# Kernel optimization log

Hardware: AMD Instinct MI355X
Metric: run time of the kernel (lower is better)

Reference implementation:

```python
import jax, jax.numpy as jnp
import numpy as np

N_VAR = 100000
N_CON = 100000
N_EDGE = 2000000
C = 32  # all channel widths


def _linear(x, W, b):
    return x @ W.T + b


def setup_inputs() -> dict:
    key = jax.random.key(0)
    ks = jax.random.split(key, 16)
    s = 1.0 / np.sqrt(C)
    se = 1.0 / np.sqrt(3 * C)
    inp = {
        "var_f": jax.random.normal(ks[0], (N_VAR, C), jnp.float32),
        "con_f": jax.random.normal(ks[1], (N_CON, C), jnp.float32),
        "combined_edge_f": jax.random.normal(ks[2], (N_EDGE, C), jnp.float32),
        "edge_index_var_con": jax.random.randint(ks[3], (2, N_EDGE), 0, N_VAR, jnp.int32),
        # var_compress_mlp
        "Wv1": jax.random.uniform(ks[4], (C, C), jnp.float32, -s, s),
        "bv1": jnp.zeros((C,), jnp.float32),
        "Wv2": jax.random.uniform(ks[5], (C, C), jnp.float32, -s, s),
        "bv2": jnp.zeros((C,), jnp.float32),
        # con_compress_mlp
        "Wc1": jax.random.uniform(ks[6], (C, C), jnp.float32, -s, s),
        "bc1": jnp.zeros((C,), jnp.float32),
        "Wc2": jax.random.uniform(ks[7], (C, C), jnp.float32, -s, s),
        "bc2": jnp.zeros((C,), jnp.float32),
        # edge_mlp (input width = 3*C)
        "We1": jax.random.uniform(ks[8], (C, 3 * C), jnp.float32, -se, se),
        "be1": jnp.zeros((C,), jnp.float32),
        "We2": jax.random.uniform(ks[9], (C, C), jnp.float32, -s, s),
        "be2": jnp.zeros((C,), jnp.float32),
    }
    return inp


def reference(var_f, con_f, combined_edge_f, edge_index_var_con,
              Wv1, bv1, Wv2, bv2, Wc1, bc1, Wc2, bc2, We1, be1, We2, be2):
    # compress node features with 2-layer ReLU MLPs (done on nodes, not edges)
    v = jax.nn.relu(_linear(jax.nn.relu(_linear(var_f, Wv1, bv1)), Wv2, bv2))
    c = jax.nn.relu(_linear(jax.nn.relu(_linear(con_f, Wc1, bc1)), Wc2, bc2))
    # gather per-edge and concat: [E, 3C]
    out = jnp.concatenate(
        [combined_edge_f, v[edge_index_var_con[0]], c[edge_index_var_con[1]]], axis=1)
    # edge MLP: Linear -> ReLU -> Linear (no final ReLU)
    return _linear(jax.nn.relu(_linear(out, We1, be1)), We2, be2)
```

## Files before the change

### kernel.cpp

```cpp
#include <hip/hip_runtime.h>

typedef float  f32x2  __attribute__((ext_vector_type(2)));
typedef float  f32x4  __attribute__((ext_vector_type(4)));
typedef float  f32x16 __attribute__((ext_vector_type(16)));
typedef short  s16x4  __attribute__((ext_vector_type(4)));
typedef short  s16x8  __attribute__((ext_vector_type(8)));
typedef unsigned int u32x2 __attribute__((ext_vector_type(2)));

__device__ __forceinline__ unsigned f2bf(float f) {
    unsigned u = __builtin_bit_cast(unsigned, f);
    u += 0x7FFFu + ((u >> 16) & 1u);
    return u >> 16;
}
__device__ __forceinline__ s16x4 pack4(float a, float b, float c, float d) {
    u32x2 u;
    u[0] = f2bf(a) | (f2bf(b) << 16);
    u[1] = f2bf(c) | (f2bf(d) << 16);
    return __builtin_bit_cast(s16x4, u);
}
__device__ __forceinline__ s16x4 pack4v(f32x4 v) { return pack4(v[0], v[1], v[2], v[3]); }
__device__ __forceinline__ s16x4 lo4(s16x8 v) { return __builtin_shufflevector(v, v, 0, 1, 2, 3); }
__device__ __forceinline__ s16x4 hi4(s16x8 v) { return __builtin_shufflevector(v, v, 4, 5, 6, 7); }

__device__ __forceinline__ void node_body(
    const float* __restrict__ X,
    const float* __restrict__ W1, const float* __restrict__ b1,
    const float* __restrict__ W2, const float* __restrict__ b2,
    const float* __restrict__ Wm, const float* __restrict__ bm,
    unsigned short* __restrict__ outp, int N, int tile0)
{
    const int lane = threadIdx.x & 63;
    const int g = lane >> 5, m = lane & 31;
    const int ntile = (N + 31) >> 5;
    if (tile0 >= ntile) return;

    s16x4 a1[4], a2[4], am[4];
#pragma unroll
    for (int q = 0; q < 4; ++q) {
        const float* p1 = W1 + m * 32 + 8 * q + 4 * g;
        a1[q] = pack4(p1[0], p1[1], p1[2], p1[3]);
        const float* p2 = W2 + m * 32 + 8 * q + 4 * g;
        a2[q] = pack4(p2[0], p2[1], p2[2], p2[3]);
        const float* pm = Wm + m * 96 + 8 * q + 4 * g;
        am[q] = pack4(pm[0], pm[1], pm[2], pm[3]);
    }
    f32x16 f1, f2, f3;
#pragma unroll
    for (int r = 0; r < 16; ++r) {
        int ch = (r & 3) + 8 * (r >> 2) + 4 * g;
        f1[r] = b1[ch];
        f2[r] = b2[ch];
        f3[r] = bm ? bm[ch] : 0.f;
    }

#pragma unroll
    for (int k = 0; k < 4; ++k) {
        const int tile = tile0 + k;
        if (tile >= ntile) break;
        const int node0 = tile * 32 + m;
        const int node = node0 < N ? node0 : N - 1;

        s16x4 bX[4];
#pragma unroll
        for (int q = 0; q < 4; ++q) {
            f32x4 v = *reinterpret_cast<const f32x4*>(X + (size_t)node * 32 + 8 * q + 4 * g);
            bX[q] = pack4v(v);
        }
        f32x16 acc = f1;
#pragma unroll
        for (int q = 0; q < 4; ++q) acc = __builtin_amdgcn_mfma_f32_32x32x8bf16_1k(a1[q], bX[q], acc, 0, 0, 0);
        s16x4 bH[4];
#pragma unroll
        for (int q = 0; q < 4; ++q)
            bH[q] = pack4(fmaxf(acc[4*q+0], 0.f), fmaxf(acc[4*q+1], 0.f),
                          fmaxf(acc[4*q+2], 0.f), fmaxf(acc[4*q+3], 0.f));
        acc = f2;
#pragma unroll
        for (int q = 0; q < 4; ++q) acc = __builtin_amdgcn_mfma_f32_32x32x8bf16_1k(a2[q], bH[q], acc, 0, 0, 0);
#pragma unroll
        for (int q = 0; q < 4; ++q)
            bH[q] = pack4(fmaxf(acc[4*q+0], 0.f), fmaxf(acc[4*q+1], 0.f),
                          fmaxf(acc[4*q+2], 0.f), fmaxf(acc[4*q+3], 0.f));
        acc = f3;
#pragma unroll
        for (int q = 0; q < 4; ++q) acc = __builtin_amdgcn_mfma_f32_32x32x8bf16_1k(am[q], bH[q], acc, 0, 0, 0);

        if (node0 < N) {
#pragma unroll
            for (int q = 0; q < 4; ++q) {
                s16x4 o = pack4(acc[4*q+0], acc[4*q+1], acc[4*q+2], acc[4*q+3]);
                *reinterpret_cast<s16x4*>(outp + (size_t)node0 * 32 + 8 * q + 4 * g) = o;
            }
        }
    }
}

__global__ __launch_bounds__(256) void nodes_kernel(
    const float* __restrict__ var_f, const float* __restrict__ con_f,
    const float* __restrict__ Wv1, const float* __restrict__ bv1,
    const float* __restrict__ Wv2, const float* __restrict__ bv2,
    const float* __restrict__ Wc1, const float* __restrict__ bc1,
    const float* __restrict__ Wc2, const float* __restrict__ bc2,
    const float* __restrict__ We1, const float* __restrict__ be1,
    unsigned short* __restrict__ pv, unsigned short* __restrict__ pc,
    int nV, int nC, int wavesV)
{
    const int wvg = (blockIdx.x * blockDim.x + threadIdx.x) >> 6;
    if (wvg < wavesV) {
        node_body(var_f, Wv1, bv1, Wv2, bv2, We1 + 32, be1, pv, nV, wvg * 4);
    } else {
        node_body(con_f, Wc1, bc1, Wc2, bc2, We1 + 64, nullptr, pc, nC,
                  (wvg - wavesV) * 4);
    }
}

__global__ __launch_bounds__(256, 4) void edge_kernel(
    const float* __restrict__ Ef, const int* __restrict__ idx,
    const unsigned short* __restrict__ pv, const unsigned short* __restrict__ pc,
    const float* __restrict__ We1, const float* __restrict__ We2,
    const float* __restrict__ be2,
    float* __restrict__ out, int nE)
{
    const int lane = threadIdx.x & 63;
    const int m = lane & 15, c = lane >> 4;

    s16x4 aW1[2][2], aP[2][2], aW2[2][2];
    f32x4 b2f[2];
#pragma unroll
    for (int r = 0; r < 2; ++r) {
#pragma unroll
        for (int kk = 0; kk < 2; ++kk) {
            const float* p1 = We1 + (16 * r + m) * 96 + 16 * kk + 4 * c;
            aW1[r][kk] = pack4(p1[0], p1[1], p1[2], p1[3]);
            const float* p2 = We2 + (16 * r + m) * 32 + 16 * kk + 4 * c;
            aW2[r][kk] = pack4(p2[0], p2[1], p2[2], p2[3]);
            const int j_hit = 16 * r + m - 8 * c - 4 * kk;
            s16x4 w;
#pragma unroll
            for (int j = 0; j < 4; ++j) w[j] = (short)((j == j_hit) ? 0x3F80 : 0);
            aP[r][kk] = w;
        }
        f32x4 b;
#pragma unroll
        for (int j = 0; j < 4; ++j) b[j] = be2[16 * r + 4 * c + j];
        b2f[r] = b;
    }

    const int ntile = nE >> 5;
    const int nw = (gridDim.x * blockDim.x) >> 6;
    int t = (blockIdx.x * blockDim.x + threadIdx.x) >> 6;
    if (t >= ntile) return;

    int ib0[2], ib1[2];
    s16x4 ebf[2][2];
    s16x8 pvf[2], pcf[2];
    {
        int i0[2], i1[2];
#pragma unroll
        for (int e = 0; e < 2; ++e) {
            i0[e] = idx[t * 32 + 16 * e + m];
            i1[e] = idx[nE + t * 32 + 16 * e + m];
        }
#pragma unroll
        for (int e = 0; e < 2; ++e) {
#pragma unroll
            for (int kk = 0; kk < 2; ++kk) {
                f32x4 v = *reinterpret_cast<const f32x4*>(
                    Ef + (size_t)(t * 32 + 16 * e + m) * 32 + 16 * kk + 4 * c);
                ebf[e][kk] = pack4v(v);
            }
            pvf[e] = *reinterpret_cast<const s16x8*>(pv + (size_t)i0[e] * 32 + 8 * c);
            pcf[e] = *reinterpret_cast<const s16x8*>(pc + (size_t)i1[e] * 32 + 8 * c);
        }
        int t1 = (t + nw < ntile) ? t + nw : t;
#pragma unroll
        for (int e = 0; e < 2; ++e) {
            ib0[e] = idx[t1 * 32 + 16 * e + m];
            ib1[e] = idx[nE + t1 * 32 + 16 * e + m];
        }
    }

    while (true) {
        const int tn = t + nw;
        const int tc = tn < ntile ? tn : t;

        f32x4 nef[2][2];
        s16x8 npv[2], npc[2];
        int ic0[2], ic1[2];
#pragma unroll
        for (int e = 0; e < 2; ++e) {
#pragma unroll
            for (int kk = 0; kk < 2; ++kk)
                nef[e][kk] = *reinterpret_cast<const f32x4*>(
                    Ef + (size_t)(tc * 32 + 16 * e + m) * 32 + 16 * kk + 4 * c);
            npv[e] = *reinterpret_cast<const s16x8*>(pv + (size_t)ib0[e] * 32 + 8 * c);
            npc[e] = *reinterpret_cast<const s16x8*>(pc + (size_t)ib1[e] * 32 + 8 * c);
        }
        {
            int t2 = (tn + nw < ntile) ? tn + nw : tc;
#pragma unroll
            for (int e = 0; e < 2; ++e) {
                ic0[e] = idx[t2 * 32 + 16 * e + m];
                ic1[e] = idx[nE + t2 * 32 + 16 * e + m];
            }
        }

        f32x4 a00 = {}, a01 = {}, a10 = {}, a11 = {};
        a00 = __builtin_amdgcn_mfma_f32_16x16x16bf16_1k(aW1[0][0], ebf[0][0], a00, 0, 0, 0);
        a01 = __builtin_amdgcn_mfma_f32_16x16x16bf16_1k(aW1[0][0], ebf[1][0], a01, 0, 0, 0);
        a10 = __builtin_amdgcn_mfma_f32_16x16x16bf16_1k(aW1[1][0], ebf[0][0], a10, 0, 0, 0);
        a11 = __builtin_amdgcn_mfma_f32_16x16x16bf16_1k(aW1[1][0], ebf[1][0], a11, 0, 0, 0);
        a00 = __builtin_amdgcn_mfma_f32_16x16x16bf16_1k(aW1[0][1], ebf[0][1], a00, 0, 0, 0);
        a01 = __builtin_amdgcn_mfma_f32_16x16x16bf16_1k(aW1[0][1], ebf[1][1], a01, 0, 0, 0);
        a10 = __builtin_amdgcn_mfma_f32_16x16x16bf16_1k(aW1[1][1], ebf[0][1], a10, 0, 0, 0);
        a11 = __builtin_amdgcn_mfma_f32_16x16x16bf16_1k(aW1[1][1], ebf[1][1], a11, 0, 0, 0);
        a00 = __builtin_amdgcn_mfma_f32_16x16x16bf16_1k(aP[0][0], lo4(pvf[0]), a00, 0, 0, 0);
        a00 = __builtin_amdgcn_mfma_f32_16x16x16bf16_1k(aP[0][1], hi4(pvf[0]), a00, 0, 0, 0);
        a01 = __builtin_amdgcn_mfma_f32_16x16x16bf16_1k(aP[0][0], lo4(pvf[1]), a01, 0, 0, 0);
        a01 = __builtin_amdgcn_mfma_f32_16x16x16bf16_1k(aP[0][1], hi4(pvf[1]), a01, 0, 0, 0);
        a10 = __builtin_amdgcn_mfma_f32_16x16x16bf16_1k(aP[1][0], lo4(pvf[0]), a10, 0, 0, 0);
        a10 = __builtin_amdgcn_mfma_f32_16x16x16bf16_1k(aP[1][1], hi4(pvf[0]), a10, 0, 0, 0);
        a11 = __builtin_amdgcn_mfma_f32_16x16x16bf16_1k(aP[1][0], lo4(pvf[1]), a11, 0, 0, 0);
        a11 = __builtin_amdgcn_mfma_f32_16x16x16bf16_1k(aP[1][1], hi4(pvf[1]), a11, 0, 0, 0);
        a00 = __builtin_amdgcn_mfma_f32_16x16x16bf16_1k(aP[0][0], lo4(pcf[0]), a00, 0, 0, 0);
        a00 = __builtin_amdgcn_mfma_f32_16x16x16bf16_1k(aP[0][1], hi4(pcf[0]), a00, 0, 0, 0);
        a01 = __builtin_amdgcn_mfma_f32_16x16x16bf16_1k(aP[0][0], lo4(pcf[1]), a01, 0, 0, 0);
        a01 = __builtin_amdgcn_mfma_f32_16x16x16bf16_1k(aP[0][1], hi4(pcf[1]), a01, 0, 0, 0);
        a10 = __builtin_amdgcn_mfma_f32_16x16x16bf16_1k(aP[1][0], lo4(pcf[0]), a10, 0, 0, 0);
        a10 = __builtin_amdgcn_mfma_f32_16x16x16bf16_1k(aP[1][1], hi4(pcf[0]), a10, 0, 0, 0);
        a11 = __builtin_amdgcn_mfma_f32_16x16x16bf16_1k(aP[1][0], lo4(pcf[1]), a11, 0, 0, 0);
        a11 = __builtin_amdgcn_mfma_f32_16x16x16bf16_1k(aP[1][1], hi4(pcf[1]), a11, 0, 0, 0);

        s16x4 bH00 = pack4(fmaxf(a00[0], 0.f), fmaxf(a00[1], 0.f), fmaxf(a00[2], 0.f), fmaxf(a00[3], 0.f));
        s16x4 bH01 = pack4(fmaxf(a10[0], 0.f), fmaxf(a10[1], 0.f), fmaxf(a10[2], 0.f), fmaxf(a10[3], 0.f));
        s16x4 bH10 = pack4(fmaxf(a01[0], 0.f), fmaxf(a01[1], 0.f), fmaxf(a01[2], 0.f), fmaxf(a01[3], 0.f));
        s16x4 bH11 = pack4(fmaxf(a11[0], 0.f), fmaxf(a11[1], 0.f), fmaxf(a11[2], 0.f), fmaxf(a11[3], 0.f));

        f32x4 o00 = b2f[0], o01 = b2f[0], o10 = b2f[1], o11 = b2f[1];
        o00 = __builtin_amdgcn_mfma_f32_16x16x16bf16_1k(aW2[0][0], bH00, o00, 0, 0, 0);
        o01 = __builtin_amdgcn_mfma_f32_16x16x16bf16_1k(aW2[0][0], bH10, o01, 0, 0, 0);
        o10 = __builtin_amdgcn_mfma_f32_16x16x16bf16_1k(aW2[1][0], bH00, o10, 0, 0, 0);
        o11 = __builtin_amdgcn_mfma_f32_16x16x16bf16_1k(aW2[1][0], bH10, o11, 0, 0, 0);
        o00 = __builtin_amdgcn_mfma_f32_16x16x16bf16_1k(aW2[0][1], bH01, o00, 0, 0, 0);
        o01 = __builtin_amdgcn_mfma_f32_16x16x16bf16_1k(aW2[0][1], bH11, o01, 0, 0, 0);
        o10 = __builtin_amdgcn_mfma_f32_16x16x16bf16_1k(aW2[1][1], bH01, o10, 0, 0, 0);
        o11 = __builtin_amdgcn_mfma_f32_16x16x16bf16_1k(aW2[1][1], bH11, o11, 0, 0, 0);

        {
            float* obase = out + (size_t)(t * 32) * 32;
            __builtin_nontemporal_store(o00, reinterpret_cast<f32x4*>(obase + (16 * 0 + m) * 32 + 16 * 0 + 4 * c));
            __builtin_nontemporal_store(o10, reinterpret_cast<f32x4*>(obase + (16 * 0 + m) * 32 + 16 * 1 + 4 * c));
            __builtin_nontemporal_store(o01, reinterpret_cast<f32x4*>(obase + (16 * 1 + m) * 32 + 16 * 0 + 4 * c));
            __builtin_nontemporal_store(o11, reinterpret_cast<f32x4*>(obase + (16 * 1 + m) * 32 + 16 * 1 + 4 * c));
        }

        if (tn >= ntile) break;
        t = tn;
#pragma unroll
        for (int e = 0; e < 2; ++e) {
#pragma unroll
            for (int kk = 0; kk < 2; ++kk) ebf[e][kk] = pack4v(nef[e][kk]);
            pvf[e] = npv[e]; pcf[e] = npc[e];
            ib0[e] = ic0[e]; ib1[e] = ic1[e];
        }
    }
}

extern "C" void kernel_launch(void* const* d_in, const int* in_sizes, int n_in,
                              void* d_out, int out_size, void* d_ws, size_t ws_size,
                              hipStream_t stream) {
    const float* var_f = (const float*)d_in[0];
    const float* con_f = (const float*)d_in[1];
    const float* Ef    = (const float*)d_in[2];
    const int*   idx   = (const int*)d_in[3];
    const float* Wv1 = (const float*)d_in[4];
    const float* bv1 = (const float*)d_in[5];
    const float* Wv2 = (const float*)d_in[6];
    const float* bv2 = (const float*)d_in[7];
    const float* Wc1 = (const float*)d_in[8];
    const float* bc1 = (const float*)d_in[9];
    const float* Wc2 = (const float*)d_in[10];
    const float* bc2 = (const float*)d_in[11];
    const float* We1 = (const float*)d_in[12];
    const float* be1 = (const float*)d_in[13];
    const float* We2 = (const float*)d_in[14];
    const float* be2 = (const float*)d_in[15];
    float* out = (float*)d_out;

    const int nV = in_sizes[0] / 32;
    const int nC = in_sizes[1] / 32;
    const int nE = in_sizes[2] / 32;

    unsigned short* pv = (unsigned short*)d_ws;
    unsigned short* pc = pv + (size_t)nV * 32;

    const int wavesV = (((nV + 31) >> 5) + 3) >> 2;
    const int wavesC = (((nC + 31) >> 5) + 3) >> 2;
    const int nodeBlocks = (wavesV + wavesC + 3) / 4;
    nodes_kernel<<<nodeBlocks, 256, 0, stream>>>(
        var_f, con_f, Wv1, bv1, Wv2, bv2, Wc1, bc1, Wc2, bc2,
        We1, be1, pv, pc, nV, nC, wavesV);

    edge_kernel<<<2048, 256, 0, stream>>>(Ef, idx, pv, pc, We1, We2, be2, out, nE);
}
```

Baseline: 176.3 us.

## Double-buffer edge tile prefetch two deep and stage output through LDS

The edge loop is restructured into two alternating register buffer sets, so feature and gather loads are issued two tiles ahead and index loads four tiles ahead, instead of one tile ahead. Output tiles are transposed through a padded per-wave LDS buffer so each lane writes contiguous 16-byte chunks of full rows rather than scattered fragments. The grid is halved to 1024 blocks. In exchange, register pressure rises from the doubled live prefetch state and LDS traffic is added. With fewer blocks there may be less latency hiding across waves.

After: 167.2 us. -5.2%, faster.

```diff
diff --git a/kernel.cpp b/kernel.cpp
--- a/kernel.cpp
+++ b/kernel.cpp
@@ -114,6 +114,92 @@
     }
 }
 
+#define EDGE_PHASE(P_ef00, P_ef01, P_ef10, P_ef11, P_pv0, P_pv1, P_pc0, P_pc1, \
+                   IX00, IX01, IX10, IX11, tcur)                               \
+    {                                                                          \
+        const int t_ = (tcur);                                                 \
+         \
+        s16x4 eb00 = pack4v(P_ef00), eb01 = pack4v(P_ef01);                    \
+        s16x4 eb10 = pack4v(P_ef10), eb11 = pack4v(P_ef11);                    \
+        f32x4 a00 = {}, a01 = {}, a10 = {}, a11 = {};                          \
+        a00 = __builtin_amdgcn_mfma_f32_16x16x16bf16_1k(aW1[0][0], eb00, a00, 0, 0, 0); \
+        a01 = __builtin_amdgcn_mfma_f32_16x16x16bf16_1k(aW1[0][0], eb10, a01, 0, 0, 0); \
+        a10 = __builtin_amdgcn_mfma_f32_16x16x16bf16_1k(aW1[1][0], eb00, a10, 0, 0, 0); \
+        a11 = __builtin_amdgcn_mfma_f32_16x16x16bf16_1k(aW1[1][0], eb10, a11, 0, 0, 0); \
+        a00 = __builtin_amdgcn_mfma_f32_16x16x16bf16_1k(aW1[0][1], eb01, a00, 0, 0, 0); \
+        a01 = __builtin_amdgcn_mfma_f32_16x16x16bf16_1k(aW1[0][1], eb11, a01, 0, 0, 0); \
+        a10 = __builtin_amdgcn_mfma_f32_16x16x16bf16_1k(aW1[1][1], eb01, a10, 0, 0, 0); \
+        a11 = __builtin_amdgcn_mfma_f32_16x16x16bf16_1k(aW1[1][1], eb11, a11, 0, 0, 0); \
+        a00 = __builtin_amdgcn_mfma_f32_16x16x16bf16_1k(aP[0][0], lo4(P_pv0), a00, 0, 0, 0); \
+        a00 = __builtin_amdgcn_mfma_f32_16x16x16bf16_1k(aP[0][1], hi4(P_pv0), a00, 0, 0, 0); \
+        a01 = __builtin_amdgcn_mfma_f32_16x16x16bf16_1k(aP[0][0], lo4(P_pv1), a01, 0, 0, 0); \
+        a01 = __builtin_amdgcn_mfma_f32_16x16x16bf16_1k(aP[0][1], hi4(P_pv1), a01, 0, 0, 0); \
+        a10 = __builtin_amdgcn_mfma_f32_16x16x16bf16_1k(aP[1][0], lo4(P_pv0), a10, 0, 0, 0); \
+        a10 = __builtin_amdgcn_mfma_f32_16x16x16bf16_1k(aP[1][1], hi4(P_pv0), a10, 0, 0, 0); \
+        a11 = __builtin_amdgcn_mfma_f32_16x16x16bf16_1k(aP[1][0], lo4(P_pv1), a11, 0, 0, 0); \
+        a11 = __builtin_amdgcn_mfma_f32_16x16x16bf16_1k(aP[1][1], hi4(P_pv1), a11, 0, 0, 0); \
+        a00 = __builtin_amdgcn_mfma_f32_16x16x16bf16_1k(aP[0][0], lo4(P_pc0), a00, 0, 0, 0); \
+        a00 = __builtin_amdgcn_mfma_f32_16x16x16bf16_1k(aP[0][1], hi4(P_pc0), a00, 0, 0, 0); \
+        a01 = __builtin_amdgcn_mfma_f32_16x16x16bf16_1k(aP[0][0], lo4(P_pc1), a01, 0, 0, 0); \
+        a01 = __builtin_amdgcn_mfma_f32_16x16x16bf16_1k(aP[0][1], hi4(P_pc1), a01, 0, 0, 0); \
+        a10 = __builtin_amdgcn_mfma_f32_16x16x16bf16_1k(aP[1][0], lo4(P_pc0), a10, 0, 0, 0); \
+        a10 = __builtin_amdgcn_mfma_f32_16x16x16bf16_1k(aP[1][1], hi4(P_pc0), a10, 0, 0, 0); \
+        a11 = __builtin_amdgcn_mfma_f32_16x16x16bf16_1k(aP[1][0], lo4(P_pc1), a11, 0, 0, 0); \
+        a11 = __builtin_amdgcn_mfma_f32_16x16x16bf16_1k(aP[1][1], hi4(P_pc1), a11, 0, 0, 0); \
+        s16x4 bH00 = pack4(fmaxf(a00[0], 0.f), fmaxf(a00[1], 0.f), fmaxf(a00[2], 0.f), fmaxf(a00[3], 0.f)); \
+        s16x4 bH01 = pack4(fmaxf(a10[0], 0.f), fmaxf(a10[1], 0.f), fmaxf(a10[2], 0.f), fmaxf(a10[3], 0.f)); \
+        s16x4 bH10 = pack4(fmaxf(a01[0], 0.f), fmaxf(a01[1], 0.f), fmaxf(a01[2], 0.f), fmaxf(a01[3], 0.f)); \
+        s16x4 bH11 = pack4(fmaxf(a11[0], 0.f), fmaxf(a11[1], 0.f), fmaxf(a11[2], 0.f), fmaxf(a11[3], 0.f)); \
+        f32x4 o00 = b2f[0], o01 = b2f[0], o10 = b2f[1], o11 = b2f[1];          \
+        o00 = __builtin_amdgcn_mfma_f32_16x16x16bf16_1k(aW2[0][0], bH00, o00, 0, 0, 0); \
+        o01 = __builtin_amdgcn_mfma_f32_16x16x16bf16_1k(aW2[0][0], bH10, o01, 0, 0, 0); \
+        o10 = __builtin_amdgcn_mfma_f32_16x16x16bf16_1k(aW2[1][0], bH00, o10, 0, 0, 0); \
+        o11 = __builtin_amdgcn_mfma_f32_16x16x16bf16_1k(aW2[1][0], bH10, o11, 0, 0, 0); \
+        o00 = __builtin_amdgcn_mfma_f32_16x16x16bf16_1k(aW2[0][1], bH01, o00, 0, 0, 0); \
+        o01 = __builtin_amdgcn_mfma_f32_16x16x16bf16_1k(aW2[0][1], bH11, o01, 0, 0, 0); \
+        o10 = __builtin_amdgcn_mfma_f32_16x16x16bf16_1k(aW2[1][1], bH01, o10, 0, 0, 0); \
+        o11 = __builtin_amdgcn_mfma_f32_16x16x16bf16_1k(aW2[1][1], bH11, o11, 0, 0, 0); \
+         \
+        {                                                                      \
+            int tf = t_ + 2 * nw; if (tf >= ntile) tf = ntile - 1;             \
+            P_ef00 = *reinterpret_cast<const f32x4*>(Ef + (size_t)(tf * 32 + m) * 32 + 4 * c); \
+            P_ef01 = *reinterpret_cast<const f32x4*>(Ef + (size_t)(tf * 32 + m) * 32 + 16 + 4 * c); \
+            P_ef10 = *reinterpret_cast<const f32x4*>(Ef + (size_t)(tf * 32 + 16 + m) * 32 + 4 * c); \
+            P_ef11 = *reinterpret_cast<const f32x4*>(Ef + (size_t)(tf * 32 + 16 + m) * 32 + 16 + 4 * c); \
+            P_pv0 = *reinterpret_cast<const s16x8*>(pv + (size_t)IX00 * 32 + 8 * c); \
+            P_pv1 = *reinterpret_cast<const s16x8*>(pv + (size_t)IX01 * 32 + 8 * c); \
+            P_pc0 = *reinterpret_cast<const s16x8*>(pc + (size_t)IX10 * 32 + 8 * c); \
+            P_pc1 = *reinterpret_cast<const s16x8*>(pc + (size_t)IX11 * 32 + 8 * c); \
+            int ti = t_ + 4 * nw; if (ti >= ntile) ti = ntile - 1;             \
+            IX00 = idx[ti * 32 + m];        IX01 = idx[ti * 32 + 16 + m];      \
+            IX10 = idx[nE + ti * 32 + m];   IX11 = idx[nE + ti * 32 + 16 + m]; \
+        }                                                                      \
+                \
+        {                                                                      \
+            float* p_ = ldsw + (size_t)m * 34 + 4 * c;                         \
+            *reinterpret_cast<f32x2*>(p_)      = f32x2{o00[0], o00[1]};        \
+            *reinterpret_cast<f32x2*>(p_ + 2)  = f32x2{o00[2], o00[3]};        \
+            *reinterpret_cast<f32x2*>(p_ + 16) = f32x2{o10[0], o10[1]};        \
+            *reinterpret_cast<f32x2*>(p_ + 18) = f32x2{o10[2], o10[3]};        \
+            float* q_ = ldsw + (size_t)(16 + m) * 34 + 4 * c;                  \
+            *reinterpret_cast<f32x2*>(q_)      = f32x2{o01[0], o01[1]};        \
+            *reinterpret_cast<f32x2*>(q_ + 2)  = f32x2{o01[2], o01[3]};        \
+            *reinterpret_cast<f32x2*>(q_ + 16) = f32x2{o11[0], o11[1]};        \
+            *reinterpret_cast<f32x2*>(q_ + 18) = f32x2{o11[2], o11[3]};        \
+            float* obase = out + (size_t)t_ * 1024;                            \
+            _Pragma("unroll")                                                  \
+            for (int p = 0; p < 4; ++p) {                                      \
+                int li = p * 256 + lane * 4;                                   \
+                int row = li >> 5, col = li & 31;                              \
+                const float* s_ = ldsw + (size_t)row * 34 + col;               \
+                f32x2 lo_ = *reinterpret_cast<const f32x2*>(s_);               \
+                f32x2 hi_ = *reinterpret_cast<const f32x2*>(s_ + 2);           \
+                f32x4 v_; v_[0] = lo_[0]; v_[1] = lo_[1]; v_[2] = hi_[0]; v_[3] = hi_[1]; \
+                __builtin_nontemporal_store(v_, reinterpret_cast<f32x4*>(obase + li)); \
+            }                                                                  \
+        }                                                                      \
+    }
+
 __global__ __launch_bounds__(256, 4) void edge_kernel(
     const float* __restrict__ Ef, const int* __restrict__ idx,
     const unsigned short* __restrict__ pv, const unsigned short* __restrict__ pc,
@@ -121,8 +207,11 @@
     const float* __restrict__ be2,
     float* __restrict__ out, int nE)
 {
+    __shared__ float ldso[4 * 1088];
     const int lane = threadIdx.x & 63;
+    const int wv = threadIdx.x >> 6;
     const int m = lane & 15, c = lane >> 4;
+    float* ldsw = ldso + wv * 1088;
 
     s16x4 aW1[2][2], aP[2][2], aW2[2][2];
     f32x4 b2f[2];
@@ -151,118 +240,49 @@
     int t = (blockIdx.x * blockDim.x + threadIdx.x) >> 6;
     if (t >= ntile) return;
 
-    int ib0[2], ib1[2];
-    s16x4 ebf[2][2];
-    s16x8 pvf[2], pcf[2];
+    f32x4 Aef00, Aef01, Aef10, Aef11, Bef00, Bef01, Bef10, Bef11;
+    s16x8 Apv0, Apv1, Apc0, Apc1, Bpv0, Bpv1, Bpc0, Bpc1;
+    int ia00, ia01, ia10, ia11, ib00, ib01, ib10, ib11;
     {
-        int i0[2], i1[2];
-#pragma unroll
-        for (int e = 0; e < 2; ++e) {
-            i0[e] = idx[t * 32 + 16 * e + m];
-            i1[e] = idx[nE + t * 32 + 16 * e + m];
-        }
-#pragma unroll
-        for (int e = 0; e < 2; ++e) {
-#pragma unroll
-            for (int kk = 0; kk < 2; ++kk) {
-                f32x4 v = *reinterpret_cast<const f32x4*>(
-                    Ef + (size_t)(t * 32 + 16 * e + m) * 32 + 16 * kk + 4 * c);
-                ebf[e][kk] = pack4v(v);
-            }
-            pvf[e] = *reinterpret_cast<const s16x8*>(pv + (size_t)i0[e] * 32 + 8 * c);
-            pcf[e] = *reinterpret_cast<const s16x8*>(pc + (size_t)i1[e] * 32 + 8 * c);
-        }
-        int t1 = (t + nw < ntile) ? t + nw : t;
-#pragma unroll
-        for (int e = 0; e < 2; ++e) {
-            ib0[e] = idx[t1 * 32 + 16 * e + m];
-            ib1[e] = idx[nE + t1 * 32 + 16 * e + m];
-        }
+        const int t0 = t;
+        int t1 = t + nw;     if (t1 >= ntile) t1 = ntile - 1;
+        int j000 = idx[t0 * 32 + m],      j001 = idx[t0 * 32 + 16 + m];
+        int j010 = idx[nE + t0 * 32 + m], j011 = idx[nE + t0 * 32 + 16 + m];
+        int j100 = idx[t1 * 32 + m],      j101 = idx[t1 * 32 + 16 + m];
+        int j110 = idx[nE + t1 * 32 + m], j111 = idx[nE + t1 * 32 + 16 + m];
+        Aef00 = *reinterpret_cast<const f32x4*>(Ef + (size_t)(t0 * 32 + m) * 32 + 4 * c);
+        Aef01 = *reinterpret_cast<const f32x4*>(Ef + (size_t)(t0 * 32 + m) * 32 + 16 + 4 * c);
+        Aef10 = *reinterpret_cast<const f32x4*>(Ef + (size_t)(t0 * 32 + 16 + m) * 32 + 4 * c);
+        Aef11 = *reinterpret_cast<const f32x4*>(Ef + (size_t)(t0 * 32 + 16 + m) * 32 + 16 + 4 * c);
+        Bef00 = *reinterpret_cast<const f32x4*>(Ef + (size_t)(t1 * 32 + m) * 32 + 4 * c);
+        Bef01 = *reinterpret_cast<const f32x4*>(Ef + (size_t)(t1 * 32 + m) * 32 + 16 + 4 * c);
+        Bef10 = *reinterpret_cast<const f32x4*>(Ef + (size_t)(t1 * 32 + 16 + m) * 32 + 4 * c);
+        Bef11 = *reinterpret_cast<const f32x4*>(Ef + (size_t)(t1 * 32 + 16 + m) * 32 + 16 + 4 * c);
+        Apv0 = *reinterpret_cast<const s16x8*>(pv + (size_t)j000 * 32 + 8 * c);
+        Apv1 = *reinterpret_cast<const s16x8*>(pv + (size_t)j001 * 32 + 8 * c);
+        Apc0 = *reinterpret_cast<const s16x8*>(pc + (size_t)j010 * 32 + 8 * c);
+        Apc1 = *reinterpret_cast<const s16x8*>(pc + (size_t)j011 * 32 + 8 * c);
+        Bpv0 = *reinterpret_cast<const s16x8*>(pv + (size_t)j100 * 32 + 8 * c);
+        Bpv1 = *reinterpret_cast<const s16x8*>(pv + (size_t)j101 * 32 + 8 * c);
+        Bpc0 = *reinterpret_cast<const s16x8*>(pc + (size_t)j110 * 32 + 8 * c);
+        Bpc1 = *reinterpret_cast<const s16x8*>(pc + (size_t)j111 * 32 + 8 * c);
+        int t2 = t + 2 * nw; if (t2 >= ntile) t2 = ntile - 1;
+        int t3 = t + 3 * nw; if (t3 >= ntile) t3 = ntile - 1;
+        ia00 = idx[t2 * 32 + m];      ia01 = idx[t2 * 32 + 16 + m];
+        ia10 = idx[nE + t2 * 32 + m]; ia11 = idx[nE + t2 * 32 + 16 + m];
+        ib00 = idx[t3 * 32 + m];      ib01 = idx[t3 * 32 + 16 + m];
+        ib10 = idx[nE + t3 * 32 + m]; ib11 = idx[nE + t3 * 32 + 16 + m];
     }
 
     while (true) {
-        const int tn = t + nw;
-        const int tc = tn < ntile ? tn : t;
-
-        f32x4 nef[2][2];
-        s16x8 npv[2], npc[2];
-        int ic0[2], ic1[2];
-#pragma unroll
-        for (int e = 0; e < 2; ++e) {
-#pragma unroll
-            for (int kk = 0; kk < 2; ++kk)
-                nef[e][kk] = *reinterpret_cast<const f32x4*>(
-                    Ef + (size_t)(tc * 32 + 16 * e + m) * 32 + 16 * kk + 4 * c);
-            npv[e] = *reinterpret_cast<const s16x8*>(pv + (size_t)ib0[e] * 32 + 8 * c);
-            npc[e] = *reinterpret_cast<const s16x8*>(pc + (size_t)ib1[e] * 32 + 8 * c);
-        }
-        {
-            int t2 = (tn + nw < ntile) ? tn + nw : tc;
-#pragma unroll
-            for (int e = 0; e < 2; ++e) {
-                ic0[e] = idx[t2 * 32 + 16 * e + m];
-                ic1[e] = idx[nE + t2 * 32 + 16 * e + m];
-            }
-        }
-
-        f32x4 a00 = {}, a01 = {}, a10 = {}, a11 = {};
-        a00 = __builtin_amdgcn_mfma_f32_16x16x16bf16_1k(aW1[0][0], ebf[0][0], a00, 0, 0, 0);
-        a01 = __builtin_amdgcn_mfma_f32_16x16x16bf16_1k(aW1[0][0], ebf[1][0], a01, 0, 0, 0);
-        a10 = __builtin_amdgcn_mfma_f32_16x16x16bf16_1k(aW1[1][0], ebf[0][0], a10, 0, 0, 0);
-        a11 = __builtin_amdgcn_mfma_f32_16x16x16bf16_1k(aW1[1][0], ebf[1][0], a11, 0, 0, 0);
-        a00 = __builtin_amdgcn_mfma_f32_16x16x16bf16_1k(aW1[0][1], ebf[0][1], a00, 0, 0, 0);
-        a01 = __builtin_amdgcn_mfma_f32_16x16x16bf16_1k(aW1[0][1], ebf[1][1], a01, 0, 0, 0);
-        a10 = __builtin_amdgcn_mfma_f32_16x16x16bf16_1k(aW1[1][1], ebf[0][1], a10, 0, 0, 0);
-        a11 = __builtin_amdgcn_mfma_f32_16x16x16bf16_1k(aW1[1][1], ebf[1][1], a11, 0, 0, 0);
-        a00 = __builtin_amdgcn_mfma_f32_16x16x16bf16_1k(aP[0][0], lo4(pvf[0]), a00, 0, 0, 0);
-        a00 = __builtin_amdgcn_mfma_f32_16x16x16bf16_1k(aP[0][1], hi4(pvf[0]), a00, 0, 0, 0);
-        a01 = __builtin_amdgcn_mfma_f32_16x16x16bf16_1k(aP[0][0], lo4(pvf[1]), a01, 0, 0, 0);
-        a01 = __builtin_amdgcn_mfma_f32_16x16x16bf16_1k(aP[0][1], hi4(pvf[1]), a01, 0, 0, 0);
-        a10 = __builtin_amdgcn_mfma_f32_16x16x16bf16_1k(aP[1][0], lo4(pvf[0]), a10, 0, 0, 0);
-        a10 = __builtin_amdgcn_mfma_f32_16x16x16bf16_1k(aP[1][1], hi4(pvf[0]), a10, 0, 0, 0);
-        a11 = __builtin_amdgcn_mfma_f32_16x16x16bf16_1k(aP[1][0], lo4(pvf[1]), a11, 0, 0, 0);
-        a11 = __builtin_amdgcn_mfma_f32_16x16x16bf16_1k(aP[1][1], hi4(pvf[1]), a11, 0, 0, 0);
-        a00 = __builtin_amdgcn_mfma_f32_16x16x16bf16_1k(aP[0][0], lo4(pcf[0]), a00, 0, 0, 0);
-        a00 = __builtin_amdgcn_mfma_f32_16x16x16bf16_1k(aP[0][1], hi4(pcf[0]), a00, 0, 0, 0);
-        a01 = __builtin_amdgcn_mfma_f32_16x16x16bf16_1k(aP[0][0], lo4(pcf[1]), a01, 0, 0, 0);
-        a01 = __builtin_amdgcn_mfma_f32_16x16x16bf16_1k(aP[0][1], hi4(pcf[1]), a01, 0, 0, 0);
-        a10 = __builtin_amdgcn_mfma_f32_16x16x16bf16_1k(aP[1][0], lo4(pcf[0]), a10, 0, 0, 0);
-        a10 = __builtin_amdgcn_mfma_f32_16x16x16bf16_1k(aP[1][1], hi4(pcf[0]), a10, 0, 0, 0);
-        a11 = __builtin_amdgcn_mfma_f32_16x16x16bf16_1k(aP[1][0], lo4(pcf[1]), a11, 0, 0, 0);
-        a11 = __builtin_amdgcn_mfma_f32_16x16x16bf16_1k(aP[1][1], hi4(pcf[1]), a11, 0, 0, 0);
-
-        s16x4 bH00 = pack4(fmaxf(a00[0], 0.f), fmaxf(a00[1], 0.f), fmaxf(a00[2], 0.f), fmaxf(a00[3], 0.f));
-        s16x4 bH01 = pack4(fmaxf(a10[0], 0.f), fmaxf(a10[1], 0.f), fmaxf(a10[2], 0.f), fmaxf(a10[3], 0.f));
-        s16x4 bH10 = pack4(fmaxf(a01[0], 0.f), fmaxf(a01[1], 0.f), fmaxf(a01[2], 0.f), fmaxf(a01[3], 0.f));
-        s16x4 bH11 = pack4(fmaxf(a11[0], 0.f), fmaxf(a11[1], 0.f), fmaxf(a11[2], 0.f), fmaxf(a11[3], 0.f));
-
-        f32x4 o00 = b2f[0], o01 = b2f[0], o10 = b2f[1], o11 = b2f[1];
-        o00 = __builtin_amdgcn_mfma_f32_16x16x16bf16_1k(aW2[0][0], bH00, o00, 0, 0, 0);
-        o01 = __builtin_amdgcn_mfma_f32_16x16x16bf16_1k(aW2[0][0], bH10, o01, 0, 0, 0);
-        o10 = __builtin_amdgcn_mfma_f32_16x16x16bf16_1k(aW2[1][0], bH00, o10, 0, 0, 0);
-        o11 = __builtin_amdgcn_mfma_f32_16x16x16bf16_1k(aW2[1][0], bH10, o11, 0, 0, 0);
-        o00 = __builtin_amdgcn_mfma_f32_16x16x16bf16_1k(aW2[0][1], bH01, o00, 0, 0, 0);
-        o01 = __builtin_amdgcn_mfma_f32_16x16x16bf16_1k(aW2[0][1], bH11, o01, 0, 0, 0);
-        o10 = __builtin_amdgcn_mfma_f32_16x16x16bf16_1k(aW2[1][1], bH01, o10, 0, 0, 0);
-        o11 = __builtin_amdgcn_mfma_f32_16x16x16bf16_1k(aW2[1][1], bH11, o11, 0, 0, 0);
-
-        {
-            float* obase = out + (size_t)(t * 32) * 32;
-            __builtin_nontemporal_store(o00, reinterpret_cast<f32x4*>(obase + (16 * 0 + m) * 32 + 16 * 0 + 4 * c));
-            __builtin_nontemporal_store(o10, reinterpret_cast<f32x4*>(obase + (16 * 0 + m) * 32 + 16 * 1 + 4 * c));
-            __builtin_nontemporal_store(o01, reinterpret_cast<f32x4*>(obase + (16 * 1 + m) * 32 + 16 * 0 + 4 * c));
-            __builtin_nontemporal_store(o11, reinterpret_cast<f32x4*>(obase + (16 * 1 + m) * 32 + 16 * 1 + 4 * c));
-        }
-
-        if (tn >= ntile) break;
-        t = tn;
-#pragma unroll
-        for (int e = 0; e < 2; ++e) {
-#pragma unroll
-            for (int kk = 0; kk < 2; ++kk) ebf[e][kk] = pack4v(nef[e][kk]);
-            pvf[e] = npv[e]; pcf[e] = npc[e];
-            ib0[e] = ic0[e]; ib1[e] = ic1[e];
-        }
+        EDGE_PHASE(Aef00, Aef01, Aef10, Aef11, Apv0, Apv1, Apc0, Apc1,
+                   ia00, ia01, ia10, ia11, t);
+        if (t + nw >= ntile) break;
+        t += nw;
+        EDGE_PHASE(Bef00, Bef01, Bef10, Bef11, Bpv0, Bpv1, Bpc0, Bpc1,
+                   ib00, ib01, ib10, ib11, t);
+        if (t + nw >= ntile) break;
+        t += nw;
     }
 }
 
@@ -301,5 +321,5 @@
         var_f, con_f, Wv1, bv1, Wv2, bv2, Wc1, bc1, Wc2, bc2,
         We1, be1, pv, pc, nV, nC, wavesV);
 
-    edge_kernel<<<2048, 256, 0, stream>>>(Ef, idx, pv, pc, We1, We2, be2, out, nE);
-}
+    edge_kernel<<<1024, 256, 0, stream>>>(Ef, idx, pv, pc, We1, We2, be2, out, nE);
+}
```
